# Performance work log

Hardware: AMD Instinct MI355X
Metric: run time of the kernel (lower is better)

## Reference

```python
import jax, jax.numpy as jnp
import numpy as np

N, D, E = 65536, 64, 4096


def setup_inputs() -> dict:
    key = jax.random.key(0)
    k1, k2, k3 = jax.random.split(key, 3)
    return {
        "input_data": jax.random.normal(k1, (N, D), dtype=jnp.float32),
        "codebook": jax.random.normal(k2, (E, D), dtype=jnp.float32),
        "dither": jax.random.uniform(k3, (E - 1,), dtype=jnp.float32),
        "entries": E,
    }


def _decode(frac_idx, cb):
    # linear interpolation between consecutive codebook entries
    e = cb.shape[0]
    ii = jnp.clip(jnp.floor(frac_idx), 0, e - 2).astype(jnp.int32)
    r = (frac_idx - ii.astype(frac_idx.dtype))[..., None]
    return (1.0 - r) * cb[ii] + r * cb[ii + 1]


def reference(input_data, codebook, dither, entries):
    cur = codebook[:entries]                                   # (E, D)
    # fractional_index = dither + linspace(0, E-2, E-1) == dither + arange(E-1)
    frac = dither + jnp.arange(entries - 1, dtype=dither.dtype)
    dithered_cb = _decode(frac, cur)                           # (E-1, D)
    # squared euclidean distances via expansion (same argmin as (x-c)^2 sum)
    x2 = jnp.sum(input_data * input_data, axis=1, keepdims=True)   # (N, 1)
    c2 = jnp.sum(dithered_cb * dithered_cb, axis=1)                # (E-1,)
    dist = x2 - 2.0 * (input_data @ dithered_cb.T) + c2[None, :]   # (N, E-1)
    integer_index = jnp.argmin(dist, axis=1)                       # (N,)
    quantized = _decode(integer_index.astype(input_data.dtype), dithered_cb)
    # perplexity = exp(entropy of codebook usage) over `entries` bins
    counts = jnp.zeros((entries,), dtype=jnp.float32).at[integer_index].add(1.0)
    avg_probs = counts / input_data.shape[0]
    perplexity = jnp.exp(-jnp.sum(avg_probs * jnp.log(avg_probs + 1e-10)))
    return quantized, perplexity, integer_index
```

## Files before the change

kernel.cpp:

```cpp
#include <hip/hip_runtime.h>
#include <math.h>


constexpr int D = 64;
constexpr int CHUNK = 64;
constexpr int NTILES = CHUNK / 16;
constexpr int E_PAD = 4096;
constexpr int NCH = E_PAD / CHUNK;
constexpr float TAU = 0.01f;
constexpr int NSLICE = 8;
constexpr int SLICE_E = E_PAD / NSLICE;
constexpr int BLK = 256;

typedef __attribute__((ext_vector_type(8))) short bf16x8;
typedef __attribute__((ext_vector_type(4))) float f32x4;

__device__ inline unsigned short f2bf(float x) {
  unsigned int u = __float_as_uint(x);
  u = (u + 0x7fffu + ((u >> 16) & 1u)) >> 16;
  return (unsigned short)u;
}
__device__ inline float bf2f(unsigned short h) {
  return __uint_as_float(((unsigned int)h) << 16);
}

__device__ __forceinline__ void gll16(const void* g, void* l) {
  __builtin_amdgcn_global_load_lds(
      (const __attribute__((address_space(1))) unsigned int*)g,
      (__attribute__((address_space(3))) unsigned int*)l, 16, 0, 0);
}
__device__ __forceinline__ void gll4(const void* g, void* l) {
  __builtin_amdgcn_global_load_lds(
      (const __attribute__((address_space(1))) unsigned int*)g,
      (__attribute__((address_space(3))) unsigned int*)l, 4, 0, 0);
}

__global__ __launch_bounds__(64) void build_kernel(
    const float* __restrict__ cb, const float* __restrict__ dither,
    float* __restrict__ dcb, unsigned short* __restrict__ dcbh,
    unsigned short* __restrict__ dcbl, float* __restrict__ c2h, int E, int Em1) {
  int i = blockIdx.x;
  int k = threadIdx.x;
  if (i >= Em1) {
    dcb[(size_t)i * D + k] = 0.f;
    dcbh[(size_t)i * D + k] = 0;
    dcbl[(size_t)i * D + k] = 0;
    if (k == 0) c2h[i] = 3.0e38f;
    return;
  }
  float frac = dither[i] + (float)i;
  int ii = (int)floorf(frac);
  ii = max(0, min(ii, E - 2));
  float r = frac - (float)ii;
  float v = (1.0f - r) * cb[(size_t)ii * D + k] + r * cb[(size_t)(ii + 1) * D + k];
  dcb[(size_t)i * D + k] = v;
  unsigned short h = f2bf(v);
  unsigned short l = f2bf(v - bf2f(h));
  dcbh[(size_t)i * D + k] = h;
  dcbl[(size_t)i * D + k] = l;
  float s = v * v;
#pragma unroll
  for (int off = 32; off > 0; off >>= 1) s += __shfl_down(s, off, 64);
  if (k == 0) c2h[i] = 0.5f * s;
}

__global__ __launch_bounds__(BLK, 4) void vq_mfma_kernel(
    const float* __restrict__ X, const unsigned short* __restrict__ dcbh,
    const unsigned short* __restrict__ dcbl, const float* __restrict__ c2h,
    int* __restrict__ out_i1, float* __restrict__ out_gap, int N) {
  __shared__ unsigned short s_h[2][CHUNK * D];
  __shared__ unsigned short s_l[2][CHUNK * D];
  __shared__ float s_c2[2][CHUNK];

  const int tid = threadIdx.x;
  const int lane = tid & 63;
  const int wv = tid >> 6;
  const int col = lane & 15;
  const int kg = lane >> 4;
  const int wvbase = blockIdx.x * 128 + wv * 32;

  bf16x8 ah0[2], ah1[2], al0[2], al1[2];
#pragma unroll
  for (int rg = 0; rg < 2; ++rg) {
    const float* xp = X + (size_t)(wvbase + rg * 16 + col) * D + kg * 8;
#pragma unroll
    for (int i = 0; i < 8; ++i) {
      float x0 = xp[i], x1 = xp[32 + i];
      unsigned short h0 = f2bf(x0), h1 = f2bf(x1);
      ah0[rg][i] = (short)h0; ah1[rg][i] = (short)h1;
      al0[rg][i] = (short)f2bf(x0 - bf2f(h0));
      al1[rg][i] = (short)f2bf(x1 - bf2f(h1));
    }
  }

  float b1[2][4], b2[2][4];
  int i1[2][4];
#pragma unroll
  for (int rg = 0; rg < 2; ++rg)
#pragma unroll
    for (int r = 0; r < 4; ++r) { b1[rg][r] = -3.4e38f; b2[rg][r] = -3.4e38f; i1[rg][r] = 0; }

  const int xs = col & 7;

  auto stage = [&](int ch, int buf) {
#pragma unroll
    for (int i = 0; i < 2; ++i) {
      const int u = (wv * 2 + i) * 64 + lane;
      const int e = u >> 3, g = u & 7;
      const size_t goff = (((size_t)(ch * CHUNK + e)) << 6) + ((g ^ (e & 7)) << 3);
      char* dst_h = (char*)s_h[buf] + (size_t)(wv * 2 + i) * 1024;
      char* dst_l = (char*)s_l[buf] + (size_t)(wv * 2 + i) * 1024;
      gll16(dcbh + goff, dst_h);
      gll16(dcbl + goff, dst_l);
    }
    if (wv == 0) {
      gll4(c2h + ch * CHUNK + lane, (char*)s_c2[buf]);
    }
  };

  stage(0, 0);
  __syncthreads();
  int cur = 0;

  for (int ch = 0; ch < NCH; ++ch) {
    const int ebase = ch * CHUNK;
    if (ch + 1 < NCH) stage(ch + 1, cur ^ 1);

#pragma unroll
    for (int t = 0; t < NTILES; ++t) {
      const int el = t * 16 + col;
      const char* bb = (const char*)s_h[cur] + el * 128;
      const char* ll = (const char*)s_l[cur] + el * 128;
      bf16x8 bh0 = *(const bf16x8*)(bb + ((kg ^ xs) << 4));
      bf16x8 bh1 = *(const bf16x8*)(bb + (((kg + 4) ^ xs) << 4));
      bf16x8 bl0 = *(const bf16x8*)(ll + ((kg ^ xs) << 4));
      bf16x8 bl1 = *(const bf16x8*)(ll + (((kg + 4) ^ xs) << 4));
      float hc2 = s_c2[cur][el];
      int colg = ebase + el;
#pragma unroll
      for (int rg = 0; rg < 2; ++rg) {
        f32x4 acc = {-hc2, -hc2, -hc2, -hc2};
        acc = __builtin_amdgcn_mfma_f32_16x16x32_bf16(ah0[rg], bh0, acc, 0, 0, 0);
        acc = __builtin_amdgcn_mfma_f32_16x16x32_bf16(ah1[rg], bh1, acc, 0, 0, 0);
        acc = __builtin_amdgcn_mfma_f32_16x16x32_bf16(ah0[rg], bl0, acc, 0, 0, 0);
        acc = __builtin_amdgcn_mfma_f32_16x16x32_bf16(ah1[rg], bl1, acc, 0, 0, 0);
        acc = __builtin_amdgcn_mfma_f32_16x16x32_bf16(al0[rg], bh0, acc, 0, 0, 0);
        acc = __builtin_amdgcn_mfma_f32_16x16x32_bf16(al1[rg], bh1, acc, 0, 0, 0);
#pragma unroll
        for (int r = 0; r < 4; ++r) {
          float s = acc[r];
          bool gt = s > b1[rg][r];
          b2[rg][r] = __builtin_amdgcn_fmed3f(b2[rg][r], s, b1[rg][r]);
          b1[rg][r] = fmaxf(b1[rg][r], s);
          i1[rg][r] = gt ? colg : i1[rg][r];
        }
      }
    }

    __syncthreads();
    cur ^= 1;
  }

#pragma unroll
  for (int m = 1; m < 16; m <<= 1) {
#pragma unroll
    for (int rg = 0; rg < 2; ++rg)
#pragma unroll
      for (int r = 0; r < 4; ++r) {
        float ob1 = __shfl_xor(b1[rg][r], m, 64);
        float ob2 = __shfl_xor(b2[rg][r], m, 64);
        int oi1 = __shfl_xor(i1[rg][r], m, 64);
        float loser = fminf(b1[rg][r], ob1);
        b2[rg][r] = fmaxf(fmaxf(b2[rg][r], ob2), loser);
        bool take = (ob1 > b1[rg][r]) || (ob1 == b1[rg][r] && oi1 < i1[rg][r]);
        b1[rg][r] = take ? ob1 : b1[rg][r];
        i1[rg][r] = take ? oi1 : i1[rg][r];
      }
  }
  if (col == 0) {
#pragma unroll
    for (int rg = 0; rg < 2; ++rg)
#pragma unroll
      for (int r = 0; r < 4; ++r) {
        int row = wvbase + rg * 16 + kg * 4 + r;
        out_i1[row] = i1[rg][r];
        out_gap[row] = b1[rg][r] - b2[rg][r];
      }
  }
}

__global__ __launch_bounds__(64) void finish_kernel(
    const int* __restrict__ out_i1, const float* __restrict__ out_gap,
    const float* __restrict__ dcb, float* __restrict__ outq,
    float* __restrict__ outidx, float* __restrict__ counts,
    int* __restrict__ rescue_n, int* __restrict__ rescue_list, int N) {
  const int lane = threadIdx.x;
  const int rowbase = blockIdx.x * 64;
  const int row = rowbase + lane;
  int bi = out_i1[row];
  float gap2 = 2.0f * out_gap[row];
  outidx[row] = (float)bi;
  if (gap2 < TAU) {
    int p = atomicAdd(rescue_n, 1);
    rescue_list[p] = row;
  } else {
    atomicAdd(&counts[bi], 1.0f);
  }
  for (int r = 0; r < 64; ++r) {
    int idx_r = __shfl(bi, r, 64);
    outq[(size_t)(rowbase + r) * D + lane] = dcb[(size_t)idx_r * D + lane];
  }
}

__global__ __launch_bounds__(64) void rescue_scan_kernel(
    const float* __restrict__ X, const float* __restrict__ dcb,
    const float* __restrict__ c2h, const int* __restrict__ rescue_n,
    const int* __restrict__ rescue_list,
    float* __restrict__ pd, int* __restrict__ pi) {
  const int lane = threadIdx.x;
  const int nu = (*rescue_n) * NSLICE;
  for (int u = blockIdx.x; u < nu; u += gridDim.x) {
    const int li = u >> 3;
    const int sl = u & (NSLICE - 1);
    const int row = rescue_list[li];

    const float4* xr = (const float4*)(X + (size_t)row * D);
    float4 x[16];
#pragma unroll
    for (int k = 0; k < 16; ++k) x[k] = xr[k];

    float best = 3.4e38f;
    int bidx = 0x7fffffff;
    const int e0 = sl * SLICE_E;
#pragma unroll 2
    for (int j = 0; j < SLICE_E / 64; ++j) {
      const int e = e0 + j * 64 + lane;
      const float4* cp = (const float4*)(dcb + (size_t)e * D);
      float d0 = 0.f, d1 = 0.f, d2 = 0.f, d3 = 0.f;
#pragma unroll
      for (int k = 0; k < 16; ++k) {
        float4 c = cp[k];
        d0 = fmaf(x[k].x, c.x, d0);
        d1 = fmaf(x[k].y, c.y, d1);
        d2 = fmaf(x[k].z, c.z, d2);
        d3 = fmaf(x[k].w, c.w, d3);
      }
      float d = c2h[e] - ((d0 + d1) + (d2 + d3));
      if (d < best) { best = d; bidx = e; }
    }
#pragma unroll
    for (int m = 1; m < 64; m <<= 1) {
      float od = __shfl_xor(best, m, 64);
      int oi = __shfl_xor(bidx, m, 64);
      if (od < best || (od == best && oi < bidx)) { best = od; bidx = oi; }
    }
    if (lane == 0) { pd[u] = best; pi[u] = bidx; }
  }
}

__global__ __launch_bounds__(64) void rescue_fin_kernel(
    const float* __restrict__ dcb, const int* __restrict__ rescue_n,
    const int* __restrict__ rescue_list, const float* __restrict__ pd,
    const int* __restrict__ pi, float* __restrict__ outq,
    float* __restrict__ outidx, float* __restrict__ counts) {
  const int lane = threadIdx.x;
  const int nr = *rescue_n;
  for (int li = blockIdx.x; li < nr; li += gridDim.x) {
    const int row = rescue_list[li];
    float d = (lane < NSLICE) ? pd[li * NSLICE + lane] : 3.5e38f;
    int ix = (lane < NSLICE) ? pi[li * NSLICE + lane] : 0x7fffffff;
#pragma unroll
    for (int m = 1; m < NSLICE; m <<= 1) {
      float od = __shfl_xor(d, m, 64);
      int oi = __shfl_xor(ix, m, 64);
      if (od < d || (od == d && oi < ix)) { d = od; ix = oi; }
    }
    int bfin = __shfl(ix, 0, 64);
    if (lane == 0) {
      outidx[row] = (float)bfin;
      atomicAdd(&counts[bfin], 1.0f);
    }
    outq[(size_t)row * D + lane] = dcb[(size_t)bfin * D + lane];
  }
}

__global__ __launch_bounds__(256) void vq_perp_kernel(
    const float* __restrict__ counts, float* __restrict__ out, int E, float invN) {
  __shared__ float red[4];
  float s = 0.f;
  for (int j = threadIdx.x; j < E; j += 256) {
    float p = counts[j] * invN;
    s += p * logf(p + 1e-10f);
  }
#pragma unroll
  for (int off = 32; off > 0; off >>= 1) s += __shfl_down(s, off, 64);
  int wid = threadIdx.x >> 6;
  if ((threadIdx.x & 63) == 0) red[wid] = s;
  __syncthreads();
  if (threadIdx.x == 0) {
    float t = (red[0] + red[1]) + (red[2] + red[3]);
    out[0] = expf(-t);
  }
}

static inline size_t align256(size_t x) { return (x + 255) & ~(size_t)255; }

extern "C" void kernel_launch(void* const* d_in, const int* in_sizes, int n_in,
                              void* d_out, int out_size, void* d_ws, size_t ws_size,
                              hipStream_t stream) {
  const float* X      = (const float*)d_in[0];
  const float* cb     = (const float*)d_in[1];
  const float* dither = (const float*)d_in[2];

  const int N   = in_sizes[0] / D;
  const int E   = in_sizes[1] / D;
  const int Em1 = in_sizes[2];

  char* w = (char*)d_ws;
  float* dcb            = (float*)w;          w += align256((size_t)E_PAD * D * sizeof(float));
  unsigned short* dcbh  = (unsigned short*)w; w += align256((size_t)E_PAD * D * sizeof(short));
  unsigned short* dcbl  = (unsigned short*)w; w += align256((size_t)E_PAD * D * sizeof(short));
  float* c2h            = (float*)w;          w += align256((size_t)E_PAD * sizeof(float));
  int* out_i1           = (int*)w;            w += align256((size_t)N * sizeof(int));
  float* out_gap        = (float*)w;          w += align256((size_t)N * sizeof(float));
  float* counts         = (float*)w;          w += align256((size_t)E_PAD * sizeof(float));
  int* rescue_n         = (int*)w;            w += align256(sizeof(int));
  int* rescue_list      = (int*)w;            w += align256((size_t)N * sizeof(int));
  float* pd             = (float*)w;          w += align256((size_t)N * NSLICE * sizeof(float));
  int* pi               = (int*)w;            w += align256((size_t)N * NSLICE * sizeof(int));

  float* outq   = (float*)d_out;
  float* perp   = (float*)d_out + (size_t)N * D;
  float* outidx = (float*)d_out + (size_t)N * D + 1;

  hipMemsetAsync(counts, 0, (size_t)E_PAD * sizeof(float), stream);
  hipMemsetAsync(rescue_n, 0, sizeof(int), stream);

  build_kernel<<<E_PAD, 64, 0, stream>>>(cb, dither, dcb, dcbh, dcbl, c2h, E, Em1);

  vq_mfma_kernel<<<N / 128, BLK, 0, stream>>>(X, dcbh, dcbl, c2h, out_i1, out_gap, N);

  finish_kernel<<<N / 64, 64, 0, stream>>>(out_i1, out_gap, dcb, outq, outidx, counts,
                                           rescue_n, rescue_list, N);

  rescue_scan_kernel<<<2048, 64, 0, stream>>>(X, dcb, c2h, rescue_n, rescue_list, pd, pi);

  rescue_fin_kernel<<<1024, 64, 0, stream>>>(dcb, rescue_n, rescue_list, pd, pi,
                                             outq, outidx, counts);

  vq_perp_kernel<<<1, 256, 0, stream>>>(counts, perp, E, 1.0f / (float)N);
}
```

Baseline: 177.8 us.

## Split codebook scan across two grid slices and merge top-2 in finish

The main MFMA distance kernel now launches a 2D grid in which each block scans only half of the codebook entries, giving twice as many blocks and half the serial chunk loop per block. Each slice writes its best score, index and second-best score to workspace, and the finish kernel merges the two slices to pick the argmin and compute the gap used for rescue. The point is better occupancy and load balance across CUs on the large GPU. The cost is that each row's X fragments are converted twice and the per-row partial results add extra global traffic. On ties the merge keeps slice 0, which has the smaller indices.

```diff
diff --git a/kernel.cpp b/kernel.cpp
--- a/kernel.cpp
+++ b/kernel.cpp
@@ -6,7 +6,9 @@
 constexpr int CHUNK = 64;
 constexpr int NTILES = CHUNK / 16;
 constexpr int E_PAD = 4096;
-constexpr int NCH = E_PAD / CHUNK;
+constexpr int ESLICES = 2;
+constexpr int SLICE = E_PAD / ESLICES;
+constexpr int NCH = SLICE / CHUNK;
 constexpr float TAU = 0.01f;
 constexpr int NSLICE = 8;
 constexpr int SLICE_E = E_PAD / NSLICE;
@@ -67,7 +69,8 @@
 __global__ __launch_bounds__(BLK, 4) void vq_mfma_kernel(
     const float* __restrict__ X, const unsigned short* __restrict__ dcbh,
     const unsigned short* __restrict__ dcbl, const float* __restrict__ c2h,
-    int* __restrict__ out_i1, float* __restrict__ out_gap, int N) {
+    float* __restrict__ out_b1, int* __restrict__ out_i1,
+    float* __restrict__ out_b2, int N) {
   __shared__ unsigned short s_h[2][CHUNK * D];
   __shared__ unsigned short s_l[2][CHUNK * D];
   __shared__ float s_c2[2][CHUNK];
@@ -77,6 +80,8 @@
   const int wv = tid >> 6;
   const int col = lane & 15;
   const int kg = lane >> 4;
+  const int slice = blockIdx.y;
+  const int sbase = slice * SLICE;
   const int wvbase = blockIdx.x * 128 + wv * 32;
 
   bf16x8 ah0[2], ah1[2], al0[2], al1[2];
@@ -98,7 +103,7 @@
 #pragma unroll
   for (int rg = 0; rg < 2; ++rg)
 #pragma unroll
-    for (int r = 0; r < 4; ++r) { b1[rg][r] = -3.4e38f; b2[rg][r] = -3.4e38f; i1[rg][r] = 0; }
+    for (int r = 0; r < 4; ++r) { b1[rg][r] = -3.4e38f; b2[rg][r] = -3.4e38f; i1[rg][r] = sbase; }
 
   const int xs = col & 7;
 
@@ -107,14 +112,14 @@
     for (int i = 0; i < 2; ++i) {
       const int u = (wv * 2 + i) * 64 + lane;
       const int e = u >> 3, g = u & 7;
-      const size_t goff = (((size_t)(ch * CHUNK + e)) << 6) + ((g ^ (e & 7)) << 3);
+      const size_t goff = (((size_t)(sbase + ch * CHUNK + e)) << 6) + ((g ^ (e & 7)) << 3);
       char* dst_h = (char*)s_h[buf] + (size_t)(wv * 2 + i) * 1024;
       char* dst_l = (char*)s_l[buf] + (size_t)(wv * 2 + i) * 1024;
       gll16(dcbh + goff, dst_h);
       gll16(dcbl + goff, dst_l);
     }
     if (wv == 0) {
-      gll4(c2h + ch * CHUNK + lane, (char*)s_c2[buf]);
+      gll4(c2h + sbase + ch * CHUNK + lane, (char*)s_c2[buf]);
     }
   };
 
@@ -123,7 +128,7 @@
   int cur = 0;
 
   for (int ch = 0; ch < NCH; ++ch) {
-    const int ebase = ch * CHUNK;
+    const int ebase = sbase + ch * CHUNK;
     if (ch + 1 < NCH) stage(ch + 1, cur ^ 1);
 
 #pragma unroll
@@ -183,22 +188,33 @@
 #pragma unroll
       for (int r = 0; r < 4; ++r) {
         int row = wvbase + rg * 16 + kg * 4 + r;
-        out_i1[row] = i1[rg][r];
-        out_gap[row] = b1[rg][r] - b2[rg][r];
+        size_t o = (size_t)slice * N + row;
+        out_b1[o] = b1[rg][r];
+        out_i1[o] = i1[rg][r];
+        out_b2[o] = b2[rg][r];
       }
   }
 }
 
 __global__ __launch_bounds__(64) void finish_kernel(
-    const int* __restrict__ out_i1, const float* __restrict__ out_gap,
+    const float* __restrict__ out_b1, const int* __restrict__ out_i1,
+    const float* __restrict__ out_b2,
     const float* __restrict__ dcb, float* __restrict__ outq,
     float* __restrict__ outidx, float* __restrict__ counts,
     int* __restrict__ rescue_n, int* __restrict__ rescue_list, int N) {
   const int lane = threadIdx.x;
   const int rowbase = blockIdx.x * 64;
   const int row = rowbase + lane;
-  int bi = out_i1[row];
-  float gap2 = 2.0f * out_gap[row];
+
+  float s0 = out_b1[row],        s1 = out_b1[(size_t)N + row];
+  int   e0 = out_i1[row],        e1 = out_i1[(size_t)N + row];
+  float q0 = out_b2[row],        q1 = out_b2[(size_t)N + row];
+  bool take = s1 > s0;
+  float b1c = take ? s1 : s0;
+  int bi = take ? e1 : e0;
+  float b2c = fmaxf(fmaxf(q0, q1), fminf(s0, s1));
+  float gap2 = 2.0f * (b1c - b2c);
+
   outidx[row] = (float)bi;
   if (gap2 < TAU) {
     int p = atomicAdd(rescue_n, 1);
@@ -321,8 +337,9 @@
   unsigned short* dcbh  = (unsigned short*)w; w += align256((size_t)E_PAD * D * sizeof(short));
   unsigned short* dcbl  = (unsigned short*)w; w += align256((size_t)E_PAD * D * sizeof(short));
   float* c2h            = (float*)w;          w += align256((size_t)E_PAD * sizeof(float));
-  int* out_i1           = (int*)w;            w += align256((size_t)N * sizeof(int));
-  float* out_gap        = (float*)w;          w += align256((size_t)N * sizeof(float));
+  float* out_b1         = (float*)w;          w += align256((size_t)ESLICES * N * sizeof(float));
+  int* out_i1           = (int*)w;            w += align256((size_t)ESLICES * N * sizeof(int));
+  float* out_b2         = (float*)w;          w += align256((size_t)ESLICES * N * sizeof(float));
   float* counts         = (float*)w;          w += align256((size_t)E_PAD * sizeof(float));
   int* rescue_n         = (int*)w;            w += align256(sizeof(int));
   int* rescue_list      = (int*)w;            w += align256((size_t)N * sizeof(int));
@@ -338,10 +355,11 @@
 
   build_kernel<<<E_PAD, 64, 0, stream>>>(cb, dither, dcb, dcbh, dcbl, c2h, E, Em1);
 
-  vq_mfma_kernel<<<N / 128, BLK, 0, stream>>>(X, dcbh, dcbl, c2h, out_i1, out_gap, N);
-
-  finish_kernel<<<N / 64, 64, 0, stream>>>(out_i1, out_gap, dcb, outq, outidx, counts,
-                                           rescue_n, rescue_list, N);
+  dim3 g2(N / 128, ESLICES);
+  vq_mfma_kernel<<<g2, BLK, 0, stream>>>(X, dcbh, dcbl, c2h, out_b1, out_i1, out_b2, N);
+
+  finish_kernel<<<N / 64, 64, 0, stream>>>(out_b1, out_i1, out_b2, dcb, outq, outidx,
+                                           counts, rescue_n, rescue_list, N);
 
   rescue_scan_kernel<<<2048, 64, 0, stream>>>(X, dcb, c2h, rescue_n, rescue_list, pd, pi);
 
```

Measured after the change: 175.3 us. Within noise of the previous version (-1.4%).
